# Optimization experiments

Hardware: AMD Instinct MI355X
Metric: run time of the kernel (lower is better)

The kernel has to match this reference:

```python
import jax, jax.numpy as jnp
import numpy as np

N, E = 50000, 150000
IN, HID, LAT, EF, HE = 16, 32, 16, 8, 128


def _p(k, shape, fan_in):
    return jax.random.normal(k, shape, jnp.float32) / np.float32(np.sqrt(fan_in))


def setup_inputs() -> dict:
    key = jax.random.key(0)
    ks = jax.random.split(key, 32)
    inp = {
        "x": jax.random.normal(ks[0], (N, IN), jnp.float32),
        "edge_index": jax.random.randint(ks[1], (2, E), 0, N, dtype=jnp.int64),
        "edge_attr": jax.random.uniform(ks[2], (E, EF), jnp.float32),
    }
    # per-conv params: edge-MLP (w1,b1,w2,b2), root weight, bias
    dims = {"c1": (IN, HID), "c2": (HID, HID), "cmu": (HID, LAT), "clv": (HID, LAT)}
    i = 3
    for name, (din, dout) in dims.items():
        inp[f"{name}_w1"] = _p(ks[i], (EF, HE), EF)
        inp[f"{name}_b1"] = jnp.zeros((HE,), jnp.float32)
        inp[f"{name}_w2"] = _p(ks[i + 1], (HE, din * dout), HE)
        inp[f"{name}_b2"] = jnp.zeros((din * dout,), jnp.float32)
        inp[f"{name}_root"] = _p(ks[i + 2], (din, dout), din)
        inp[f"{name}_bias"] = jnp.zeros((dout,), jnp.float32)
        i += 3
    return inp


def _nnconv(x, src, dst, ea, w1, b1, w2, b2, root, bias, din, dout, mean):
    # edge MLP -> per-edge weight matrix [E, din, dout]
    h = jax.nn.relu(ea @ w1 + b1)
    W = (h @ w2 + b2).reshape(-1, din, dout)
    # gather source features, per-edge matmul, scatter-reduce to targets
    msg = jnp.einsum('ei,eio->eo', x[src], W)  # [E, dout]
    agg = jax.ops.segment_sum(msg, dst, num_segments=x.shape[0])
    if mean:
        cnt = jax.ops.segment_sum(jnp.ones((dst.shape[0],), x.dtype), dst,
                                  num_segments=x.shape[0])
        agg = agg / jnp.maximum(cnt, 1.0)[:, None]
    return agg + x @ root + bias


def reference(x, edge_index, edge_attr,
              c1_w1, c1_b1, c1_w2, c1_b2, c1_root, c1_bias,
              c2_w1, c2_b1, c2_w2, c2_b2, c2_root, c2_bias,
              cmu_w1, cmu_b1, cmu_w2, cmu_b2, cmu_root, cmu_bias,
              clv_w1, clv_b1, clv_w2, clv_b2, clv_root, clv_bias):
    src, dst = edge_index[0], edge_index[1]
    h = jax.nn.relu(_nnconv(x, src, dst, edge_attr, c1_w1, c1_b1, c1_w2, c1_b2,
                            c1_root, c1_bias, IN, HID, True))
    h = jax.nn.relu(_nnconv(h, src, dst, edge_attr, c2_w1, c2_b1, c2_w2, c2_b2,
                            c2_root, c2_bias, HID, HID, True))
    mu = _nnconv(h, src, dst, edge_attr, cmu_w1, cmu_b1, cmu_w2, cmu_b2,
                 cmu_root, cmu_bias, HID, LAT, False)
    logvar = _nnconv(h, src, dst, edge_attr, clv_w1, clv_b1, clv_w2, clv_b2,
                     clv_root, clv_bias, HID, LAT, False)
    return mu, logvar
```

## Files before the change

kernel.cpp:

```cpp
#include <hip/hip_runtime.h>

typedef __attribute__((ext_vector_type(8))) _Float16 half8;
typedef __attribute__((ext_vector_type(4))) _Float16 half4v;
typedef __attribute__((ext_vector_type(2))) _Float16 half2v;
typedef __attribute__((ext_vector_type(4))) float f32x4;

constexpr int NN  = 50000;
constexpr int NE  = 150000;
constexpr int IN  = 16;
constexpr int HID = 32;
constexpr int LAT = 16;
constexpr int EF  = 8;
constexpr int HE  = 128;
constexpr int NTILE = NE / 16;
constexpr int HSTR  = HE + 2;

constexpr int SCB = 256;
constexpr int NSB = (NN + SCB - 1) / SCB;

__global__ void count_kernel(const int* __restrict__ dst, int* __restrict__ cnt) {
  int e = blockIdx.x * blockDim.x + threadIdx.x;
  if (e < NE) atomicAdd(&cnt[dst[e]], 1);
}

__launch_bounds__(SCB)
__global__ void scan1(const int* __restrict__ cnt, int* __restrict__ bsum) {
  __shared__ int sdata[SCB];
  const int i = blockIdx.x * SCB + threadIdx.x;
  sdata[threadIdx.x] = (i < NN) ? cnt[i] : 0;
  __syncthreads();
  for (int off = SCB / 2; off > 0; off >>= 1) {
    if (threadIdx.x < off) sdata[threadIdx.x] += sdata[threadIdx.x + off];
    __syncthreads();
  }
  if (threadIdx.x == 0) bsum[blockIdx.x] = sdata[0];
}

__launch_bounds__(SCB)
__global__ void scan2(int* __restrict__ bsum) {
  __shared__ int sdata[SCB];
  const int t = threadIdx.x;
  const int v = (t < NSB) ? bsum[t] : 0;
  sdata[t] = v;
  __syncthreads();
  for (int off = 1; off < SCB; off <<= 1) {
    int u = (t >= off) ? sdata[t - off] : 0;
    __syncthreads();
    sdata[t] += u;
    __syncthreads();
  }
  if (t < NSB) bsum[t] = sdata[t] - v;
}

__launch_bounds__(SCB)
__global__ void scan3(const int* __restrict__ cnt, const int* __restrict__ bsum,
                      int* __restrict__ rowptr, int* __restrict__ wptr) {
  __shared__ int sdata[SCB];
  const int i = blockIdx.x * SCB + threadIdx.x;
  const int t = threadIdx.x;
  const int v = (i < NN) ? cnt[i] : 0;
  sdata[t] = v;
  __syncthreads();
  for (int off = 1; off < SCB; off <<= 1) {
    int u = (t >= off) ? sdata[t - off] : 0;
    __syncthreads();
    sdata[t] += u;
    __syncthreads();
  }
  const int excl = sdata[t] - v + bsum[blockIdx.x];
  if (i < NN) {
    rowptr[i] = excl;
    wptr[i]   = excl;
  }
  if (i == NN - 1) rowptr[NN] = NE;
}

__global__ void fill_kernel(const int* __restrict__ dst, int* __restrict__ wptr,
                            int* __restrict__ epos) {
  int e = blockIdx.x * blockDim.x + threadIdx.x;
  if (e < NE) epos[e] = atomicAdd(&wptr[dst[e]], 1);
}

__global__ void swizzle_kernel(const float* __restrict__ w2, const float* __restrict__ b2,
                               _Float16* __restrict__ w2h, int DIN_, int DOUT_) {
  int idx = blockIdx.x * blockDim.x + threadIdx.x;
  int tot = HSTR * DIN_ * DOUT_;
  if (idx >= tot) return;
  int i  = idx % DIN_;
  int o  = (idx / DIN_) % DOUT_;
  int kk = idx / (DIN_ * DOUT_);
  float v = 0.0f;
  if (kk < HE)       v = w2[(size_t)kk * DIN_ * DOUT_ + i * DOUT_ + o];
  else if (kk == HE) v = b2[i * DOUT_ + o];
  w2h[idx] = (_Float16)v;
}

template <int DIN, int DOUT, bool DUAL>
__launch_bounds__(128)
__global__ void nnconv_mfma(const float* __restrict__ xin,
                            const int*   __restrict__ src,
                            const float* __restrict__ ea,
                            const float* __restrict__ w1A,
                            const float* __restrict__ b1A,
                            const float* __restrict__ w1B,
                            const float* __restrict__ b1B,
                            const _Float16* __restrict__ w2hA,
                            const _Float16* __restrict__ w2hB,
                            const int*   __restrict__ epos,
                            _Float16* __restrict__ msgA,
                            _Float16* __restrict__ msgB)
{
  constexpr int STEPS   = (DIN == 32) ? (HE + 1) : (HE + 2) / 2;
  constexpr int KKSTEP  = 32 / DIN;
  constexpr int BSTRIDE = KKSTEP * DOUT * DIN;

  __shared__ float    ea_s[64 * EF];
  __shared__ _Float16 h_s[64 * HSTR];

  const int tid = threadIdx.x;
  const int eb  = blockIdx.x * 64;

  {
    int e = eb + (tid >> 1);
    float4 v = make_float4(0.f, 0.f, 0.f, 0.f);
    if (e < NE) v = *((const float4*)(ea + (size_t)e * EF) + (tid & 1));
    ((float4*)ea_s)[tid] = v;
  }
  __syncthreads();

  auto build_h = [&](const float* __restrict__ w1, const float* __restrict__ b1) {
    const int kk = tid;
    float w1r[EF];
#pragma unroll
    for (int i = 0; i < EF; i++) w1r[i] = w1[i * HE + kk];
    const float bk = b1[kk];
#pragma unroll 4
    for (int e = 0; e < 64; e++) {
      float hv = bk;
#pragma unroll
      for (int i = 0; i < EF; i++) hv = fmaf(ea_s[e * EF + i], w1r[i], hv);
      hv = fmaxf(hv, 0.0f);
      h_s[e * HSTR + kk] = (_Float16)hv;
    }
    if (tid < 64) {
      h_s[tid * HSTR + HE]     = (_Float16)1.0f;
      h_s[tid * HSTR + HE + 1] = (_Float16)0.0f;
    }
  };

  build_h(w1A, b1A);
  __syncthreads();

  const int wave = tid >> 6;
  const int lane = tid & 63;
  const int m = lane & 15, q = lane >> 4;
  const int tg0 = blockIdx.x * 4 + wave * 2;

  const int i0 = (q * 8) % DIN;
  const int kq = (q * 8) / DIN;

  half2v xv[2][4];
#pragma unroll
  for (int t2 = 0; t2 < 2; t2++) {
    const int tg = tg0 + t2;
    if (tg < NTILE) {
      const int s = src[tg * 16 + m];
      const float4* xp = (const float4*)(xin + (size_t)s * DIN + i0);
      float4 a = xp[0], b = xp[1];
      xv[t2][0] = (half2v){(_Float16)a.x, (_Float16)a.y};
      xv[t2][1] = (half2v){(_Float16)a.z, (_Float16)a.w};
      xv[t2][2] = (half2v){(_Float16)b.x, (_Float16)b.y};
      xv[t2][3] = (half2v){(_Float16)b.z, (_Float16)b.w};
    } else {
#pragma unroll
      for (int j = 0; j < 4; j++) xv[t2][j] = (half2v){(_Float16)0.f, (_Float16)0.f};
    }
  }

  f32x4 acc[2][2];
#pragma unroll
  for (int t2 = 0; t2 < 2; t2++)
#pragma unroll
    for (int f = 0; f < 2; f++) acc[t2][f] = (f32x4){0.f, 0.f, 0.f, 0.f};

  const int hrow0 = wave * 32 + m;
  const int hrow1 = wave * 32 + 16 + m;

  if constexpr (DUAL) {
    {
      const _Float16* bp = w2hA + (size_t)(kq * DOUT + m) * DIN + i0;
#pragma unroll 4
      for (int t = 0; t < STEPS; t++) {
        const half8 bfr = *(const half8*)(bp + (size_t)t * BSTRIDE);
        const int kkidx = t * KKSTEP + kq;
#pragma unroll
        for (int t2 = 0; t2 < 2; t2++) {
          const int hrow = (t2 == 0) ? hrow0 : hrow1;
          const _Float16 hv = h_s[hrow * HSTR + kkidx];
          const half2v hb = (half2v){hv, hv};
          union { half2v h2[4]; half8 h8; } af;
#pragma unroll
          for (int j = 0; j < 4; j++) af.h2[j] = xv[t2][j] * hb;
          acc[t2][0] = __builtin_amdgcn_mfma_f32_16x16x32_f16(af.h8, bfr,
                                                              acc[t2][0], 0, 0, 0);
        }
      }
    }
    __syncthreads();
    build_h(w1B, b1B);
    __syncthreads();
    {
      const _Float16* bp = w2hB + (size_t)(kq * DOUT + m) * DIN + i0;
#pragma unroll 4
      for (int t = 0; t < STEPS; t++) {
        const half8 bfr = *(const half8*)(bp + (size_t)t * BSTRIDE);
        const int kkidx = t * KKSTEP + kq;
#pragma unroll
        for (int t2 = 0; t2 < 2; t2++) {
          const int hrow = (t2 == 0) ? hrow0 : hrow1;
          const _Float16 hv = h_s[hrow * HSTR + kkidx];
          const half2v hb = (half2v){hv, hv};
          union { half2v h2[4]; half8 h8; } af;
#pragma unroll
          for (int j = 0; j < 4; j++) af.h2[j] = xv[t2][j] * hb;
          acc[t2][1] = __builtin_amdgcn_mfma_f32_16x16x32_f16(af.h8, bfr,
                                                              acc[t2][1], 0, 0, 0);
        }
      }
    }
  } else {
    const _Float16* bp0 = w2hA + (size_t)(kq * DOUT + 0 + m) * DIN + i0;
    const _Float16* bp1 = w2hA + (size_t)(kq * DOUT + 16 + m) * DIN + i0;
#pragma unroll 4
    for (int t = 0; t < STEPS; t++) {
      const half8 bfr0 = *(const half8*)(bp0 + (size_t)t * BSTRIDE);
      const half8 bfr1 = *(const half8*)(bp1 + (size_t)t * BSTRIDE);
      const int kkidx = t * KKSTEP + kq;
#pragma unroll
      for (int t2 = 0; t2 < 2; t2++) {
        const int hrow = (t2 == 0) ? hrow0 : hrow1;
        const _Float16 hv = h_s[hrow * HSTR + kkidx];
        const half2v hb = (half2v){hv, hv};
        union { half2v h2[4]; half8 h8; } af;
#pragma unroll
        for (int j = 0; j < 4; j++) af.h2[j] = xv[t2][j] * hb;
        acc[t2][0] = __builtin_amdgcn_mfma_f32_16x16x32_f16(af.h8, bfr0,
                                                            acc[t2][0], 0, 0, 0);
        acc[t2][1] = __builtin_amdgcn_mfma_f32_16x16x32_f16(af.h8, bfr1,
                                                            acc[t2][1], 0, 0, 0);
      }
    }
  }

#pragma unroll
  for (int t2 = 0; t2 < 2; t2++) {
    const int tg = tg0 + t2;
    if (tg < NTILE) {
      const int ebase = tg * 16 + q * 4;
      const int4 ep = *(const int4*)(epos + ebase);
      const int pr[4] = {ep.x, ep.y, ep.z, ep.w};
      if (DUAL) {
#pragma unroll
        for (int r = 0; r < 4; r++) {
          msgA[(size_t)pr[r] * DOUT + m] = (_Float16)acc[t2][0][r];
          msgB[(size_t)pr[r] * DOUT + m] = (_Float16)acc[t2][1][r];
        }
      } else {
#pragma unroll
        for (int f = 0; f < 2; f++)
#pragma unroll
          for (int r = 0; r < 4; r++)
            msgA[(size_t)pr[r] * DOUT + f * 16 + m] = (_Float16)acc[t2][f][r];
      }
    }
  }
}

template <int DIN, int DOUT, bool MEAN, bool RELU>
__launch_bounds__(256)
__global__ void finish_kernel(const _Float16* __restrict__ msg,
                              const int* __restrict__ rowptr,
                              const float* __restrict__ xin,
                              const float* __restrict__ root,
                              const float* __restrict__ bias,
                              float* __restrict__ out) {
  constexpr int TPN = DOUT / 4;
  const int gid = blockIdx.x * 256 + threadIdx.x;
  const int n = gid / TPN, sub = gid % TPN;
  if (n >= NN) return;
  const int o0 = sub * 4;

  const int r0 = rowptr[n], r1 = rowptr[n + 1];
  float ax = 0.f, ay = 0.f, az = 0.f, aw = 0.f;
  for (int idx = r0; idx < r1; idx++) {
    const half4v mv = *(const half4v*)(msg + (size_t)idx * DOUT + o0);
    ax += (float)mv.x; ay += (float)mv.y; az += (float)mv.z; aw += (float)mv.w;
  }
  const float inv = MEAN ? 1.0f / fmaxf((float)(r1 - r0), 1.0f) : 1.0f;
  float vx = ax * inv + bias[o0 + 0];
  float vy = ay * inv + bias[o0 + 1];
  float vz = az * inv + bias[o0 + 2];
  float vw = aw * inv + bias[o0 + 3];
#pragma unroll
  for (int i = 0; i < DIN; i++) {
    const float xi = xin[(size_t)n * DIN + i];
    const float4 rv = *(const float4*)(root + (size_t)i * DOUT + o0);
    vx = fmaf(xi, rv.x, vx); vy = fmaf(xi, rv.y, vy);
    vz = fmaf(xi, rv.z, vz); vw = fmaf(xi, rv.w, vw);
  }
  if (RELU) {
    vx = fmaxf(vx, 0.f); vy = fmaxf(vy, 0.f);
    vz = fmaxf(vz, 0.f); vw = fmaxf(vw, 0.f);
  }
  *(float4*)(out + (size_t)n * DOUT + o0) = make_float4(vx, vy, vz, vw);
}

template <int DIN>
__launch_bounds__(256)
__global__ void finish_dual(const _Float16* __restrict__ msgA,
                            const _Float16* __restrict__ msgB,
                            const int* __restrict__ rowptr,
                            const float* __restrict__ xin,
                            const float* __restrict__ rootA,
                            const float* __restrict__ biasA,
                            const float* __restrict__ rootB,
                            const float* __restrict__ biasB,
                            float* __restrict__ outA,
                            float* __restrict__ outB) {
  constexpr int TPN = LAT / 4;
  const int gid = blockIdx.x * 256 + threadIdx.x;
  const int n = gid / TPN, sub = gid % TPN;
  if (n >= NN) return;
  const int o0 = sub * 4;

  const int r0 = rowptr[n], r1 = rowptr[n + 1];
  float a0 = 0.f, a1 = 0.f, a2 = 0.f, a3 = 0.f;
  float b0 = 0.f, b1 = 0.f, b2 = 0.f, b3 = 0.f;
  for (int idx = r0; idx < r1; idx++) {
    const half4v ma = *(const half4v*)(msgA + (size_t)idx * LAT + o0);
    const half4v mb = *(const half4v*)(msgB + (size_t)idx * LAT + o0);
    a0 += (float)ma.x; a1 += (float)ma.y; a2 += (float)ma.z; a3 += (float)ma.w;
    b0 += (float)mb.x; b1 += (float)mb.y; b2 += (float)mb.z; b3 += (float)mb.w;
  }
  float va0 = a0 + biasA[o0 + 0], va1 = a1 + biasA[o0 + 1];
  float va2 = a2 + biasA[o0 + 2], va3 = a3 + biasA[o0 + 3];
  float vb0 = b0 + biasB[o0 + 0], vb1 = b1 + biasB[o0 + 1];
  float vb2 = b2 + biasB[o0 + 2], vb3 = b3 + biasB[o0 + 3];
#pragma unroll
  for (int i = 0; i < DIN; i++) {
    const float xi = xin[(size_t)n * DIN + i];
    const float4 ra = *(const float4*)(rootA + (size_t)i * LAT + o0);
    const float4 rb = *(const float4*)(rootB + (size_t)i * LAT + o0);
    va0 = fmaf(xi, ra.x, va0); va1 = fmaf(xi, ra.y, va1);
    va2 = fmaf(xi, ra.z, va2); va3 = fmaf(xi, ra.w, va3);
    vb0 = fmaf(xi, rb.x, vb0); vb1 = fmaf(xi, rb.y, vb1);
    vb2 = fmaf(xi, rb.z, vb2); vb3 = fmaf(xi, rb.w, vb3);
  }
  *(float4*)(outA + (size_t)n * LAT + o0) = make_float4(va0, va1, va2, va3);
  *(float4*)(outB + (size_t)n * LAT + o0) = make_float4(vb0, vb1, vb2, vb3);
}

extern "C" void kernel_launch(void* const* d_in, const int* in_sizes, int n_in,
                              void* d_out, int out_size, void* d_ws, size_t ws_size,
                              hipStream_t stream) {
  const float* x  = (const float*)d_in[0];
  const int*   ei = (const int*)d_in[1];
  const float* ea = (const float*)d_in[2];
  const int* src = ei;
  const int* dst = ei + NE;

  auto P = [&](int c, int j) -> const float* {
    return (const float*)d_in[3 + c * 6 + j];
  };

  float* h1  = (float*)d_ws;
  float* h2  = h1 + (size_t)NN * HID;
  _Float16* msg = (_Float16*)(h2 + (size_t)NN * HID);
  int* cnt    = (int*)(msg + (size_t)NE * 32);
  int* rowptr = cnt + NN;
  int* wptr   = rowptr + 50004;
  int* epos   = wptr + 50004;
  int* bsum   = epos + NE;
  _Float16* w2h_c1 = (_Float16*)(bsum + 256);
  _Float16* w2h_c2 = w2h_c1 + (size_t)HSTR * 32 * 16;
  _Float16* w2h_mu = w2h_c2 + (size_t)HSTR * 32 * 32;
  _Float16* w2h_lv = w2h_mu + (size_t)HSTR * 16 * 32;

  _Float16* msgA = msg;
  _Float16* msgB = msg + (size_t)NE * 16;

  float* out_mu = (float*)d_out;
  float* out_lv = out_mu + (size_t)NN * LAT;

  hipMemsetAsync(cnt, 0, (size_t)NN * sizeof(int), stream);
  count_kernel<<<dim3((NE + 255) / 256), dim3(256), 0, stream>>>(dst, cnt);
  scan1<<<dim3(NSB), dim3(SCB), 0, stream>>>(cnt, bsum);
  scan2<<<dim3(1), dim3(SCB), 0, stream>>>(bsum);
  scan3<<<dim3(NSB), dim3(SCB), 0, stream>>>(cnt, bsum, rowptr, wptr);
  fill_kernel<<<dim3((NE + 255) / 256), dim3(256), 0, stream>>>(dst, wptr, epos);

  {
    int t1 = HSTR * 16 * 32, t2 = HSTR * 32 * 32, t3 = HSTR * 32 * 16;
    swizzle_kernel<<<dim3((t1 + 255) / 256), dim3(256), 0, stream>>>(
        P(0, 2), P(0, 3), w2h_c1, IN, HID);
    swizzle_kernel<<<dim3((t2 + 255) / 256), dim3(256), 0, stream>>>(
        P(1, 2), P(1, 3), w2h_c2, HID, HID);
    swizzle_kernel<<<dim3((t3 + 255) / 256), dim3(256), 0, stream>>>(
        P(2, 2), P(2, 3), w2h_mu, HID, LAT);
    swizzle_kernel<<<dim3((t3 + 255) / 256), dim3(256), 0, stream>>>(
        P(3, 2), P(3, 3), w2h_lv, HID, LAT);
  }

  const dim3 egrid((NTILE + 3) / 4), eblk(128);

  nnconv_mfma<IN, HID, false><<<egrid, eblk, 0, stream>>>(
      x, src, ea, P(0, 0), P(0, 1), nullptr, nullptr, w2h_c1, nullptr,
      epos, msg, nullptr);
  finish_kernel<IN, HID, true, true>
      <<<dim3((NN * (HID / 4) + 255) / 256), dim3(256), 0, stream>>>(
          msg, rowptr, x, P(0, 4), P(0, 5), h1);

  nnconv_mfma<HID, HID, false><<<egrid, eblk, 0, stream>>>(
      h1, src, ea, P(1, 0), P(1, 1), nullptr, nullptr, w2h_c2, nullptr,
      epos, msg, nullptr);
  finish_kernel<HID, HID, true, true>
      <<<dim3((NN * (HID / 4) + 255) / 256), dim3(256), 0, stream>>>(
          msg, rowptr, h1, P(1, 4), P(1, 5), h2);

  nnconv_mfma<HID, LAT, true><<<egrid, eblk, 0, stream>>>(
      h2, src, ea, P(2, 0), P(2, 1), P(3, 0), P(3, 1), w2h_mu, w2h_lv,
      epos, msgA, msgB);
  finish_dual<HID>
      <<<dim3((NN * (LAT / 4) + 255) / 256), dim3(256), 0, stream>>>(
          msgA, msgB, rowptr, h2, P(2, 4), P(2, 5), P(3, 4), P(3, 5),
          out_mu, out_lv);
}
```

Measured before the change: 401.1 us.

## Process four edge tiles per wave and vectorize hidden-activation LDS reads

Each block now covers 128 edges, and each wave handles 4 tiles of 16 edges instead of 2. This reuses every loaded W2 B-fragment across twice as many MFMAs, roughly halving global weight traffic per edge. The hidden-layer reads from LDS become 8-wide vector loads per chunk instead of scalar per-step loads. The constant-one bias column is replaced by an explicit tail MFMA step. The cost is more registers for accumulators and x fragments, double the LDS per block, and half as many blocks, which may lower occupancy.

```diff
diff --git a/kernel.cpp b/kernel.cpp
--- a/kernel.cpp
+++ b/kernel.cpp
@@ -17,6 +17,12 @@
 
 constexpr int SCB = 256;
 constexpr int NSB = (NN + SCB - 1) / SCB;
+
+union XU {
+  half2v h2[4];
+  half8  h8;
+  _Float16 h[8];
+};
 
 __global__ void count_kernel(const int* __restrict__ dst, int* __restrict__ cnt) {
   int e = blockIdx.x * blockDim.x + threadIdx.x;
@@ -110,21 +116,27 @@
                             _Float16* __restrict__ msgA,
                             _Float16* __restrict__ msgB)
 {
-  constexpr int STEPS   = (DIN == 32) ? (HE + 1) : (HE + 2) / 2;
   constexpr int KKSTEP  = 32 / DIN;
+  constexpr int CHS     = 8 / KKSTEP;
   constexpr int BSTRIDE = KKSTEP * DOUT * DIN;
-
-  __shared__ float    ea_s[64 * EF];
-  __shared__ _Float16 h_s[64 * HSTR];
+  constexpr int HS      = 136;
+  constexpr int TILES   = 4;
+
+  __shared__ float    ea_s[128 * EF];
+  __shared__ _Float16 h_s[128 * HS];
 
   const int tid = threadIdx.x;
-  const int eb  = blockIdx.x * 64;
+  const int eb  = blockIdx.x * 128;
 
   {
-    int e = eb + (tid >> 1);
-    float4 v = make_float4(0.f, 0.f, 0.f, 0.f);
-    if (e < NE) v = *((const float4*)(ea + (size_t)e * EF) + (tid & 1));
-    ((float4*)ea_s)[tid] = v;
+    const int e = eb + tid;
+    float4 v0 = make_float4(0.f, 0.f, 0.f, 0.f), v1 = v0;
+    if (e < NE) {
+      const float4* p = (const float4*)(ea + (size_t)e * EF);
+      v0 = p[0]; v1 = p[1];
+    }
+    float4* qp = (float4*)&ea_s[tid * EF];
+    qp[0] = v0; qp[1] = v1;
   }
   __syncthreads();
 
@@ -135,16 +147,16 @@
     for (int i = 0; i < EF; i++) w1r[i] = w1[i * HE + kk];
     const float bk = b1[kk];
 #pragma unroll 4
-    for (int e = 0; e < 64; e++) {
+    for (int e = 0; e < 128; e++) {
+      const float4* p = (const float4*)&ea_s[e * EF];
+      const float4 a = p[0], b = p[1];
       float hv = bk;
-#pragma unroll
-      for (int i = 0; i < EF; i++) hv = fmaf(ea_s[e * EF + i], w1r[i], hv);
+      hv = fmaf(a.x, w1r[0], hv); hv = fmaf(a.y, w1r[1], hv);
+      hv = fmaf(a.z, w1r[2], hv); hv = fmaf(a.w, w1r[3], hv);
+      hv = fmaf(b.x, w1r[4], hv); hv = fmaf(b.y, w1r[5], hv);
+      hv = fmaf(b.z, w1r[6], hv); hv = fmaf(b.w, w1r[7], hv);
       hv = fmaxf(hv, 0.0f);
-      h_s[e * HSTR + kk] = (_Float16)hv;
-    }
-    if (tid < 64) {
-      h_s[tid * HSTR + HE]     = (_Float16)1.0f;
-      h_s[tid * HSTR + HE + 1] = (_Float16)0.0f;
+      h_s[e * HS + kk] = (_Float16)hv;
     }
   };
 
@@ -154,107 +166,147 @@
   const int wave = tid >> 6;
   const int lane = tid & 63;
   const int m = lane & 15, q = lane >> 4;
-  const int tg0 = blockIdx.x * 4 + wave * 2;
-
   const int i0 = (q * 8) % DIN;
   const int kq = (q * 8) / DIN;
-
-  half2v xv[2][4];
-#pragma unroll
-  for (int t2 = 0; t2 < 2; t2++) {
-    const int tg = tg0 + t2;
+  const int tg0 = blockIdx.x * 8 + wave * TILES;
+
+  XU xv[TILES];
+#pragma unroll
+  for (int t = 0; t < TILES; t++) {
+    const int tg = tg0 + t;
     if (tg < NTILE) {
       const int s = src[tg * 16 + m];
       const float4* xp = (const float4*)(xin + (size_t)s * DIN + i0);
-      float4 a = xp[0], b = xp[1];
-      xv[t2][0] = (half2v){(_Float16)a.x, (_Float16)a.y};
-      xv[t2][1] = (half2v){(_Float16)a.z, (_Float16)a.w};
-      xv[t2][2] = (half2v){(_Float16)b.x, (_Float16)b.y};
-      xv[t2][3] = (half2v){(_Float16)b.z, (_Float16)b.w};
+      const float4 a = xp[0], b = xp[1];
+      xv[t].h2[0] = (half2v){(_Float16)a.x, (_Float16)a.y};
+      xv[t].h2[1] = (half2v){(_Float16)a.z, (_Float16)a.w};
+      xv[t].h2[2] = (half2v){(_Float16)b.x, (_Float16)b.y};
+      xv[t].h2[3] = (half2v){(_Float16)b.z, (_Float16)b.w};
     } else {
 #pragma unroll
-      for (int j = 0; j < 4; j++) xv[t2][j] = (half2v){(_Float16)0.f, (_Float16)0.f};
-    }
-  }
-
-  f32x4 acc[2][2];
-#pragma unroll
-  for (int t2 = 0; t2 < 2; t2++)
-#pragma unroll
-    for (int f = 0; f < 2; f++) acc[t2][f] = (f32x4){0.f, 0.f, 0.f, 0.f};
-
-  const int hrow0 = wave * 32 + m;
-  const int hrow1 = wave * 32 + 16 + m;
+      for (int j = 0; j < 4; j++) xv[t].h2[j] = (half2v){(_Float16)0.f, (_Float16)0.f};
+    }
+  }
+
+  f32x4 acc[TILES][2];
+#pragma unroll
+  for (int t = 0; t < TILES; t++)
+#pragma unroll
+    for (int f = 0; f < 2; f++) acc[t][f] = (f32x4){0.f, 0.f, 0.f, 0.f};
+
+  int hrow[TILES];
+#pragma unroll
+  for (int t = 0; t < TILES; t++) hrow[t] = wave * 64 + t * 16 + m;
+
+  auto make_af = [&](const XU& xvt, _Float16 hv) -> XU {
+    const half2v hb = (half2v){hv, hv};
+    XU af;
+#pragma unroll
+    for (int j = 0; j < 4; j++) af.h2[j] = xvt.h2[j] * hb;
+    return af;
+  };
 
   if constexpr (DUAL) {
-    {
-      const _Float16* bp = w2hA + (size_t)(kq * DOUT + m) * DIN + i0;
-#pragma unroll 4
-      for (int t = 0; t < STEPS; t++) {
-        const half8 bfr = *(const half8*)(bp + (size_t)t * BSTRIDE);
-        const int kkidx = t * KKSTEP + kq;
-#pragma unroll
-        for (int t2 = 0; t2 < 2; t2++) {
-          const int hrow = (t2 == 0) ? hrow0 : hrow1;
-          const _Float16 hv = h_s[hrow * HSTR + kkidx];
-          const half2v hb = (half2v){hv, hv};
-          union { half2v h2[4]; half8 h8; } af;
-#pragma unroll
-          for (int j = 0; j < 4; j++) af.h2[j] = xv[t2][j] * hb;
-          acc[t2][0] = __builtin_amdgcn_mfma_f32_16x16x32_f16(af.h8, bfr,
-                                                              acc[t2][0], 0, 0, 0);
+    auto run_pass = [&](const _Float16* __restrict__ bp, const int f) {
+#pragma unroll 1
+      for (int c = 0; c < 16; c++) {
+        XU hc[TILES];
+#pragma unroll
+        for (int t = 0; t < TILES; t++)
+          hc[t].h8 = *(const half8*)&h_s[hrow[t] * HS + c * 8];
+#pragma unroll
+        for (int s = 0; s < CHS; s++) {
+          const half8 bf = *(const half8*)(bp + (size_t)(c * CHS + s) * BSTRIDE);
+#pragma unroll
+          for (int t = 0; t < TILES; t++) {
+            _Float16 hv;
+            if (DIN == 32) hv = hc[t].h[s];
+            else {
+              const _Float16 h0 = hc[t].h[2 * s], h1 = hc[t].h[2 * s + 1];
+              hv = kq ? h1 : h0;
+            }
+            const XU af = make_af(xv[t], hv);
+            acc[t][f] = __builtin_amdgcn_mfma_f32_16x16x32_f16(af.h8, bf,
+                                                               acc[t][f], 0, 0, 0);
+          }
         }
       }
-    }
-    __syncthreads();
-    build_h(w1B, b1B);
-    __syncthreads();
-    {
-      const _Float16* bp = w2hB + (size_t)(kq * DOUT + m) * DIN + i0;
-#pragma unroll 4
-      for (int t = 0; t < STEPS; t++) {
-        const half8 bfr = *(const half8*)(bp + (size_t)t * BSTRIDE);
-        const int kkidx = t * KKSTEP + kq;
-#pragma unroll
-        for (int t2 = 0; t2 < 2; t2++) {
-          const int hrow = (t2 == 0) ? hrow0 : hrow1;
-          const _Float16 hv = h_s[hrow * HSTR + kkidx];
-          const half2v hb = (half2v){hv, hv};
-          union { half2v h2[4]; half8 h8; } af;
-#pragma unroll
-          for (int j = 0; j < 4; j++) af.h2[j] = xv[t2][j] * hb;
-          acc[t2][1] = __builtin_amdgcn_mfma_f32_16x16x32_f16(af.h8, bfr,
-                                                              acc[t2][1], 0, 0, 0);
+      {
+        const half8 bf = *(const half8*)(bp + (size_t)(128 / KKSTEP) * BSTRIDE);
+#pragma unroll
+        for (int t = 0; t < TILES; t++) {
+          XU af;
+          if (DIN == 32) af = xv[t];
+          else {
+#pragma unroll
+            for (int j = 0; j < 4; j++)
+              af.h2[j] = kq ? (half2v){(_Float16)0.f, (_Float16)0.f} : xv[t].h2[j];
+          }
+          acc[t][f] = __builtin_amdgcn_mfma_f32_16x16x32_f16(af.h8, bf,
+                                                             acc[t][f], 0, 0, 0);
         }
       }
-    }
+    };
+
+    const _Float16* bpA = w2hA + (size_t)(kq * DOUT + m) * DIN + i0;
+    const _Float16* bpB = w2hB + (size_t)(kq * DOUT + m) * DIN + i0;
+    run_pass(bpA, 0);
+    __syncthreads();
+    build_h(w1B, b1B);
+    __syncthreads();
+    run_pass(bpB, 1);
   } else {
     const _Float16* bp0 = w2hA + (size_t)(kq * DOUT + 0 + m) * DIN + i0;
     const _Float16* bp1 = w2hA + (size_t)(kq * DOUT + 16 + m) * DIN + i0;
-#pragma unroll 4
-    for (int t = 0; t < STEPS; t++) {
-      const half8 bfr0 = *(const half8*)(bp0 + (size_t)t * BSTRIDE);
-      const half8 bfr1 = *(const half8*)(bp1 + (size_t)t * BSTRIDE);
-      const int kkidx = t * KKSTEP + kq;
-#pragma unroll
-      for (int t2 = 0; t2 < 2; t2++) {
-        const int hrow = (t2 == 0) ? hrow0 : hrow1;
-        const _Float16 hv = h_s[hrow * HSTR + kkidx];
-        const half2v hb = (half2v){hv, hv};
-        union { half2v h2[4]; half8 h8; } af;
-#pragma unroll
-        for (int j = 0; j < 4; j++) af.h2[j] = xv[t2][j] * hb;
-        acc[t2][0] = __builtin_amdgcn_mfma_f32_16x16x32_f16(af.h8, bfr0,
-                                                            acc[t2][0], 0, 0, 0);
-        acc[t2][1] = __builtin_amdgcn_mfma_f32_16x16x32_f16(af.h8, bfr1,
-                                                            acc[t2][1], 0, 0, 0);
+#pragma unroll 1
+    for (int c = 0; c < 16; c++) {
+      XU hc[TILES];
+#pragma unroll
+      for (int t = 0; t < TILES; t++)
+        hc[t].h8 = *(const half8*)&h_s[hrow[t] * HS + c * 8];
+#pragma unroll
+      for (int s = 0; s < CHS; s++) {
+        const half8 bf0 = *(const half8*)(bp0 + (size_t)(c * CHS + s) * BSTRIDE);
+        const half8 bf1 = *(const half8*)(bp1 + (size_t)(c * CHS + s) * BSTRIDE);
+#pragma unroll
+        for (int t = 0; t < TILES; t++) {
+          _Float16 hv;
+          if (DIN == 32) hv = hc[t].h[s];
+          else {
+            const _Float16 h0 = hc[t].h[2 * s], h1 = hc[t].h[2 * s + 1];
+            hv = kq ? h1 : h0;
+          }
+          const XU af = make_af(xv[t], hv);
+          acc[t][0] = __builtin_amdgcn_mfma_f32_16x16x32_f16(af.h8, bf0,
+                                                             acc[t][0], 0, 0, 0);
+          acc[t][1] = __builtin_amdgcn_mfma_f32_16x16x32_f16(af.h8, bf1,
+                                                             acc[t][1], 0, 0, 0);
+        }
       }
     }
-  }
-
-#pragma unroll
-  for (int t2 = 0; t2 < 2; t2++) {
-    const int tg = tg0 + t2;
+    {
+      const half8 bf0 = *(const half8*)(bp0 + (size_t)(128 / KKSTEP) * BSTRIDE);
+      const half8 bf1 = *(const half8*)(bp1 + (size_t)(128 / KKSTEP) * BSTRIDE);
+#pragma unroll
+      for (int t = 0; t < TILES; t++) {
+        XU af;
+        if (DIN == 32) af = xv[t];
+        else {
+#pragma unroll
+          for (int j = 0; j < 4; j++)
+            af.h2[j] = kq ? (half2v){(_Float16)0.f, (_Float16)0.f} : xv[t].h2[j];
+        }
+        acc[t][0] = __builtin_amdgcn_mfma_f32_16x16x32_f16(af.h8, bf0,
+                                                           acc[t][0], 0, 0, 0);
+        acc[t][1] = __builtin_amdgcn_mfma_f32_16x16x32_f16(af.h8, bf1,
+                                                           acc[t][1], 0, 0, 0);
+      }
+    }
+  }
+
+#pragma unroll
+  for (int t = 0; t < TILES; t++) {
+    const int tg = tg0 + t;
     if (tg < NTILE) {
       const int ebase = tg * 16 + q * 4;
       const int4 ep = *(const int4*)(epos + ebase);
@@ -262,15 +314,15 @@
       if (DUAL) {
 #pragma unroll
         for (int r = 0; r < 4; r++) {
-          msgA[(size_t)pr[r] * DOUT + m] = (_Float16)acc[t2][0][r];
-          msgB[(size_t)pr[r] * DOUT + m] = (_Float16)acc[t2][1][r];
+          msgA[(size_t)pr[r] * DOUT + m] = (_Float16)acc[t][0][r];
+          msgB[(size_t)pr[r] * DOUT + m] = (_Float16)acc[t][1][r];
         }
       } else {
 #pragma unroll
         for (int f = 0; f < 2; f++)
 #pragma unroll
           for (int r = 0; r < 4; r++)
-            msgA[(size_t)pr[r] * DOUT + f * 16 + m] = (_Float16)acc[t2][f][r];
+            msgA[(size_t)pr[r] * DOUT + f * 16 + m] = (_Float16)acc[t][f][r];
       }
     }
   }
@@ -411,7 +463,7 @@
         P(3, 2), P(3, 3), w2h_lv, HID, LAT);
   }
 
-  const dim3 egrid((NTILE + 3) / 4), eblk(128);
+  const dim3 egrid((NTILE + 7) / 8), eblk(128);
 
   nnconv_mfma<IN, HID, false><<<egrid, eblk, 0, stream>>>(
       x, src, ea, P(0, 0), P(0, 1), nullptr, nullptr, w2h_c1, nullptr,
```

Result: faster. 362.3 us (-9.7%).
